# Kernel optimization log

Measured on AMD Instinct MI355X. Metric: run time of the kernel, lower is better.

## Reference

```python
import jax, jax.numpy as jnp
import numpy as np


def setup_inputs() -> dict:
    key = jax.random.key(0)
    ks = jax.random.split(key, 5)
    B, N, C = 64, 384, 768
    return {
        "x": jax.random.normal(ks[0], (B, N, C), dtype=jnp.float32),
        "x_hsi": jax.random.normal(ks[1], (B, N, C), dtype=jnp.float32),
        "qkv_w": jax.random.normal(ks[2], (3 * C, C), dtype=jnp.float32) * 0.02,
        "proj_w": jax.random.normal(ks[3], (C, C), dtype=jnp.float32) * 0.02,
        "proj_b": jax.random.normal(ks[4], (C,), dtype=jnp.float32) * 0.02,
        "t_h": 8,
        "t_w": 8,
        "s_h": 16,
        "s_w": 16,
        "num_heads": 12,
    }


def reference(x, x_hsi, qkv_w, proj_w, proj_b, t_h, t_w, s_h, s_w, num_heads):
    B, N, C = x.shape
    H = num_heads
    Dh = C // H
    scale = Dh ** -0.5
    Lt = t_h * t_w * 2  # template tokens (2 templates)

    def qkv_heads(inp):
        qkv = (inp @ qkv_w.T).reshape(B, N, 3, H, Dh)
        qkv = jnp.transpose(qkv, (2, 0, 3, 1, 4))  # [3,B,H,N,Dh]
        return qkv[0], qkv[1], qkv[2]

    q, k, v = qkv_heads(x)
    q_hsi, k_hsi, v_hsi = qkv_heads(x_hsi)

    q_mt, q_s = q[:, :, :Lt], q[:, :, Lt:]
    k_mt, v_mt = k[:, :, :Lt], v[:, :, :Lt]
    q_s_hsi = q_hsi[:, :, Lt:]

    def attn(qq, kk, vv):
        a = jax.nn.softmax(jnp.einsum('bhqd,bhkd->bhqk', qq, kk) * scale, axis=-1)
        o = jnp.einsum('bhqk,bhkd->bhqd', a, vv)
        return jnp.transpose(o, (0, 2, 1, 3)).reshape(B, -1, C)

    x_mt = attn(q_mt, k_mt, v_mt)        # template-template
    x_s = attn(q_s, k, v)                # search attends to all
    x_s_hsi = attn(q_s_hsi, k_hsi, v_hsi)  # hsi search attends to all hsi

    out = jnp.concatenate([x_mt, x_s], axis=1) @ proj_w.T + proj_b
    out_hsi = jnp.concatenate([x_mt, x_s_hsi], axis=1) @ proj_w.T + proj_b
    return out, out_hsi
```

## Files before the change

kernel.cpp:

```cpp
#include <hip/hip_runtime.h>

typedef __attribute__((ext_vector_type(8))) short short8;
typedef __attribute__((ext_vector_type(4))) short bf16x4;
typedef __attribute__((ext_vector_type(4))) float f32x4;

__device__ __forceinline__ f32x4 mfma16(short8 a, short8 b, f32x4 c) {
  return __builtin_amdgcn_mfma_f32_16x16x32_bf16(a, b, c, 0, 0, 0);
}

__device__ __forceinline__ short f2bf(float f) {
  union { float f; unsigned u; } v; v.f = f;
  unsigned r = (v.u + 0x7fffu + ((v.u >> 16) & 1u)) >> 16;
  return (short)r;
}

__device__ __forceinline__ void gload16(const short* g, short* l) {
  __builtin_amdgcn_global_load_lds(
      (const __attribute__((address_space(1))) void*)g,
      (__attribute__((address_space(3))) void*)l, 16, 0, 0);
}

__global__ __launch_bounds__(256) void cvt_k(const float* __restrict__ src,
                                             short* __restrict__ dst, long n8) {
  long i = (long)blockIdx.x * 256 + threadIdx.x;
  const long stride = (long)gridDim.x * 256;
  for (; i < n8; i += stride) {
    float4 a = *(const float4*)(src + i * 8);
    float4 b = *(const float4*)(src + i * 8 + 4);
    short8 o = {f2bf(a.x), f2bf(a.y), f2bf(a.z), f2bf(a.w),
                f2bf(b.x), f2bf(b.y), f2bf(b.z), f2bf(b.w)};
    *(short8*)(dst + i * 8) = o;
  }
}

__global__ __launch_bounds__(256) void gemm_qkv_k(
    const short* __restrict__ A0, const short* __restrict__ A1,
    const short* __restrict__ W,
    short* __restrict__ O0, short* __restrict__ O1) {
  __shared__ __align__(16) short As[128 * 32];
  __shared__ __align__(16) short Bs[128 * 32];
  const int tid = threadIdx.x;
  const int lane = tid & 63, wv = tid >> 6;
  const int l15 = lane & 15, q4 = lane >> 4;
  const int m0 = blockIdx.x * 128, n0 = blockIdx.y * 128;
  const short* A = blockIdx.z ? A1 : A0;
  short* O = blockIdx.z ? O1 : O0;
  const int wm = wv & 1, wn = wv >> 1;

  const int s0 = tid, s1 = tid + 256;
  const long ga0 = (long)(m0 + (s0 >> 2)) * 768 + (s0 & 3) * 8;
  const long ga1 = (long)(m0 + (s1 >> 2)) * 768 + (s1 & 3) * 8;
  const long gb0 = (long)(n0 + (s0 >> 2)) * 768 + (s0 & 3) * 8;
  const long gb1 = (long)(n0 + (s1 >> 2)) * 768 + (s1 & 3) * 8;
  short* lA0 = &As[(wv * 64) * 8];
  short* lA1 = &As[(wv * 64 + 256) * 8];
  short* lB0 = &Bs[(wv * 64) * 8];
  short* lB1 = &Bs[(wv * 64 + 256) * 8];

  f32x4 acc[4][4] = {};
  for (int k0 = 0; k0 < 768; k0 += 32) {
    __syncthreads();
    gload16(A + ga0 + k0, lA0);
    gload16(A + ga1 + k0, lA1);
    gload16(W + gb0 + k0, lB0);
    gload16(W + gb1 + k0, lB1);
    __syncthreads();
    short8 af[4], bf[4];
#pragma unroll
    for (int i = 0; i < 4; ++i)
      af[i] = *(const short8*)&As[(wm * 64 + i * 16 + l15) * 32 + q4 * 8];
#pragma unroll
    for (int j = 0; j < 4; ++j)
      bf[j] = *(const short8*)&Bs[(wn * 64 + j * 16 + l15) * 32 + q4 * 8];
#pragma unroll
    for (int i = 0; i < 4; ++i)
#pragma unroll
      for (int j = 0; j < 4; ++j)
        acc[i][j] = mfma16(af[i], bf[j], acc[i][j]);
  }
#pragma unroll
  for (int i = 0; i < 4; ++i)
#pragma unroll
    for (int j = 0; j < 4; ++j) {
      const int col = n0 + wn * 64 + j * 16 + l15;
#pragma unroll
      for (int r = 0; r < 4; ++r) {
        const int row = m0 + wm * 64 + i * 16 + q4 * 4 + r;
        O[(long)row * 2304 + col] = f2bf(acc[i][j][r]);
      }
    }
}

template <int NK>
__global__ __launch_bounds__(256) void attn_k(
    const short* __restrict__ qkvx, const short* __restrict__ qkvh,
    short* __restrict__ omt, short* __restrict__ os, short* __restrict__ osh) {
  constexpr int NT = NK / 16;
  constexpr int KT = NK / 64;
  constexpr int T = (NK == 128) ? 2 : 8;
  __shared__ __align__(16) short kv[2][64 * 72];
  __shared__ __align__(16) short sp[2][4][16 * 72];

  const int tid = threadIdx.x, lane = tid & 63, wv = tid >> 6;
  const int l15 = lane & 15, q4 = lane >> 4;
  const int bx = blockIdx.x;
  const int b = bx / (12 * T);
  const int rr = bx % (12 * T);
  const int h = rr / T, t = rr % T;

  const short* src;
  short* outb;
  int q0;
  if (NK == 128) {
    src = qkvx;
    outb = omt + ((long)b * 128 + t * 64) * 768 + h * 64;
    q0 = t * 64;
  } else {
    const int tt = t & 3;
    const bool hs = t >= 4;
    src = hs ? qkvh : qkvx;
    outb = (hs ? osh : os) + ((long)b * 256 + tt * 64) * 768 + h * 64;
    q0 = 128 + tt * 64;
  }
  const short* qb = src + ((long)(b * 384 + q0 + wv * 16)) * 2304 + h * 64;
  const short* kb = src + (long)b * 384 * 2304 + 768 + h * 64;
  const short* vb = kb + 768;

  const int key0 = tid >> 3, dg0 = tid & 7;
  const int key1 = key0 + 32, dg1 = dg0;

  short8 qf0 = *(const short8*)(qb + (long)l15 * 2304 + q4 * 8);
  short8 qf1 = *(const short8*)(qb + (long)l15 * 2304 + 32 + q4 * 8);

  f32x4 sacc[NT] = {};
  short8 ka0 = *(const short8*)(kb + (long)key0 * 2304 + dg0 * 8);
  short8 ka1 = *(const short8*)(kb + (long)key1 * 2304 + dg1 * 8);
#pragma unroll
  for (int kt = 0; kt < KT; ++kt) {
    const int buf = kt & 1;
    *(short8*)&kv[buf][key0 * 72 + dg0 * 8] = ka0;
    *(short8*)&kv[buf][key1 * 72 + dg1 * 8] = ka1;
    __syncthreads();
    if (kt + 1 < KT) {
      ka0 = *(const short8*)(kb + (long)((kt + 1) * 64 + key0) * 2304 + dg0 * 8);
      ka1 = *(const short8*)(kb + (long)((kt + 1) * 64 + key1) * 2304 + dg1 * 8);
    }
#pragma unroll
    for (int j = 0; j < 4; ++j) {
      short8 kf0 = *(const short8*)&kv[buf][(j * 16 + l15) * 72 + q4 * 8];
      short8 kf1 = *(const short8*)&kv[buf][(j * 16 + l15) * 72 + 32 + q4 * 8];
      sacc[kt * 4 + j] = mfma16(qf0, kf0, sacc[kt * 4 + j]);
      sacc[kt * 4 + j] = mfma16(qf1, kf1, sacc[kt * 4 + j]);
    }
  }

  short8 va0 = *(const short8*)(vb + (long)key0 * 2304 + dg0 * 8);
  short8 va1 = *(const short8*)(vb + (long)key1 * 2304 + dg1 * 8);

  const float scale = 0.125f;
  float mx[4] = {-3e38f, -3e38f, -3e38f, -3e38f};
#pragma unroll
  for (int nt = 0; nt < NT; ++nt)
#pragma unroll
    for (int r = 0; r < 4; ++r) mx[r] = fmaxf(mx[r], sacc[nt][r]);
#pragma unroll
  for (int r = 0; r < 4; ++r) {
    mx[r] = fmaxf(mx[r], __shfl_xor(mx[r], 1));
    mx[r] = fmaxf(mx[r], __shfl_xor(mx[r], 2));
    mx[r] = fmaxf(mx[r], __shfl_xor(mx[r], 4));
    mx[r] = fmaxf(mx[r], __shfl_xor(mx[r], 8));
  }
  float sm[4] = {0.f, 0.f, 0.f, 0.f};
  unsigned pb[NT][2];
#pragma unroll
  for (int nt = 0; nt < NT; ++nt) {
    float ev[4];
#pragma unroll
    for (int r = 0; r < 4; ++r) {
      ev[r] = __expf((sacc[nt][r] - mx[r]) * scale);
      sm[r] += ev[r];
    }
    pb[nt][0] = (unsigned)(unsigned short)f2bf(ev[0]) |
                ((unsigned)(unsigned short)f2bf(ev[1]) << 16);
    pb[nt][1] = (unsigned)(unsigned short)f2bf(ev[2]) |
                ((unsigned)(unsigned short)f2bf(ev[3]) << 16);
  }
#pragma unroll
  for (int r = 0; r < 4; ++r) {
    sm[r] += __shfl_xor(sm[r], 1);
    sm[r] += __shfl_xor(sm[r], 2);
    sm[r] += __shfl_xor(sm[r], 4);
    sm[r] += __shfl_xor(sm[r], 8);
  }

  f32x4 oacc[4] = {};
#pragma unroll
  for (int kt = 0; kt < KT; ++kt) {
    const int buf = kt & 1;
    char* vt = (char*)&kv[buf][0];
#pragma unroll
    for (int e = 0; e < 8; ++e) {
      const int d0 = dg0 * 8 + e;
      *(short*)(vt + ((d0 * 144 + key0 * 2) ^ (dg0 << 4))) = va0[e];
      *(short*)(vt + ((d0 * 144 + key1 * 2) ^ (dg1 << 4))) = va1[e];
    }
    short* spw = &sp[buf][wv][0];
#pragma unroll
    for (int nt2 = 0; nt2 < 4; ++nt2) {
#pragma unroll
      for (int p = 0; p < 2; ++p) {
        const unsigned w = pb[kt * 4 + nt2][p];
        spw[(q4 * 4 + 2 * p) * 72 + nt2 * 16 + l15] = (short)(w & 0xffffu);
        spw[(q4 * 4 + 2 * p + 1) * 72 + nt2 * 16 + l15] = (short)(w >> 16);
      }
    }
    __syncthreads();
    if (kt + 1 < KT) {
      va0 = *(const short8*)(vb + (long)((kt + 1) * 64 + key0) * 2304 + dg0 * 8);
      va1 = *(const short8*)(vb + (long)((kt + 1) * 64 + key1) * 2304 + dg1 * 8);
    }
#pragma unroll
    for (int ks = 0; ks < 2; ++ks) {
      short8 pf = *(const short8*)&sp[buf][wv][l15 * 72 + ks * 32 + q4 * 8];
#pragma unroll
      for (int n2 = 0; n2 < 4; ++n2) {
        const int db = n2 * 16 + l15;
        short8 vf = *(const short8*)(vt + ((db * 144 + (ks * 32 + q4 * 8) * 2) ^
                                           (((db >> 3) & 7) << 4)));
        oacc[n2] = mfma16(pf, vf, oacc[n2]);
      }
    }
  }

  short* ob = outb + wv * 16 * 768;
#pragma unroll
  for (int r = 0; r < 4; ++r) {
    const float inv = 1.f / sm[r];
#pragma unroll
    for (int n2 = 0; n2 < 4; ++n2)
      ob[(q4 * 4 + r) * 768 + n2 * 16 + l15] = f2bf(oacc[n2][r] * inv);
  }
}

__global__ __launch_bounds__(256) void gemm_proj_k(
    const short* __restrict__ mt, const short* __restrict__ sA,
    const short* __restrict__ sh,
    const short* __restrict__ W, const float* __restrict__ bias,
    float* __restrict__ out, int cb0) {
  __shared__ __align__(16) short As[128 * 32];
  __shared__ __align__(16) short Bs[128 * 32];
  const int tid = threadIdx.x;
  const int lane = tid & 63, wv = tid >> 6;
  const int l15 = lane & 15, q4 = lane >> 4;
  const int m0 = blockIdx.x * 128, n0 = blockIdx.y * 128;
  const short* s = blockIdx.z ? sh : sA;
  const int wm = wv & 1, wn = wv >> 1;

  const int s0 = tid, s1 = tid + 256;
  const int r0 = s0 >> 2, c0 = (s0 & 3) * 8;
  const int r1 = s1 >> 2, c1 = (s1 & 3) * 8;
  const int ra = m0 + r0, rb = m0 + r1;
  const int ba_ = ra / 384, na = ra % 384;
  const int bb_ = rb / 384, nb = rb % 384;
  const short* ap0 = ((na < 128) ? (mt + ((long)ba_ * 128 + na) * 768)
                                 : (s + ((long)ba_ * 256 + (na - 128)) * 768)) + c0;
  const short* ap1 = ((nb < 128) ? (mt + ((long)bb_ * 128 + nb) * 768)
                                 : (s + ((long)bb_ * 256 + (nb - 128)) * 768)) + c1;
  const short* bp0 = W + (long)(n0 + r0) * 768 + c0;
  const short* bp1 = W + (long)(n0 + r1) * 768 + c1;
  short* lA0 = &As[(wv * 64) * 8];
  short* lA1 = &As[(wv * 64 + 256) * 8];
  short* lB0 = &Bs[(wv * 64) * 8];
  short* lB1 = &Bs[(wv * 64 + 256) * 8];

  f32x4 acc[4][4] = {};
  for (int k0 = 0; k0 < 768; k0 += 32) {
    __syncthreads();
    gload16(ap0 + k0, lA0);
    gload16(ap1 + k0, lA1);
    gload16(bp0 + k0, lB0);
    gload16(bp1 + k0, lB1);
    __syncthreads();
    short8 af[4], bf[4];
#pragma unroll
    for (int i = 0; i < 4; ++i)
      af[i] = *(const short8*)&As[(wm * 64 + i * 16 + l15) * 32 + q4 * 8];
#pragma unroll
    for (int j = 0; j < 4; ++j)
      bf[j] = *(const short8*)&Bs[(wn * 64 + j * 16 + l15) * 32 + q4 * 8];
#pragma unroll
    for (int i = 0; i < 4; ++i)
#pragma unroll
      for (int j = 0; j < 4; ++j)
        acc[i][j] = mfma16(af[i], bf[j], acc[i][j]);
  }
#pragma unroll
  for (int j = 0; j < 4; ++j) {
    const int col = n0 + wn * 64 + j * 16 + l15;
    const float bvv = bias[col];
#pragma unroll
    for (int i = 0; i < 4; ++i)
#pragma unroll
      for (int r = 0; r < 4; ++r) {
        const int row = m0 + wm * 64 + i * 16 + q4 * 4 + r;
        out[(long)blockIdx.z * 18874368 + ((long)cb0 * 384 + row) * 768 + col] =
            acc[i][j][r] + bvv;
      }
  }
}

extern "C" void kernel_launch(void* const* d_in, const int* in_sizes, int n_in,
                              void* d_out, int out_size, void* d_ws, size_t ws_size,
                              hipStream_t stream) {
  (void)in_sizes; (void)n_in; (void)out_size;
  const float* x  = (const float*)d_in[0];
  const float* xh = (const float*)d_in[1];
  const float* qw = (const float*)d_in[2];
  const float* pw = (const float*)d_in[3];
  const float* pb = (const float*)d_in[4];
  float* out = (float*)d_out;

  const long qwSz = 2304L * 768 * 2;
  const long pwSz = 768L * 768 * 2;
  const long fixedW = qwSz + pwSz;
  const long perBatch = (2L * 384 * 768 + 2L * 384 * 2304 + 640L * 768) * 2;
  int CB = 64;
  while (CB > 1 && (long)CB * perBatch + fixedW > (long)ws_size) CB >>= 1;

  char* ws = (char*)d_ws;
  short* qwbf = (short*)ws;
  short* pwbf = (short*)(ws + qwSz);
  char* dyn = ws + fixedW;
  const long xbfSz = (long)CB * 384 * 768 * 2;
  const long qkvSz = (long)CB * 384 * 2304 * 2;
  const long mtSz  = (long)CB * 128 * 768 * 2;
  const long sSz   = (long)CB * 256 * 768 * 2;
  short* xbf  = (short*)dyn;
  short* xhbf = (short*)(dyn + xbfSz);
  short* qkvx = (short*)(dyn + 2 * xbfSz);
  short* qkvh = (short*)(dyn + 2 * xbfSz + qkvSz);
  short* amt  = (short*)(dyn + 2 * xbfSz + 2 * qkvSz);
  short* as_  = (short*)(dyn + 2 * xbfSz + 2 * qkvSz + mtSz);
  short* ash  = (short*)(dyn + 2 * xbfSz + 2 * qkvSz + mtSz + sSz);

  cvt_k<<<864, 256, 0, stream>>>(qw, qwbf, 2304L * 768 / 8);
  cvt_k<<<288, 256, 0, stream>>>(pw, pwbf, 768L * 768 / 8);

  const int nch = 64 / CB;
  for (int c = 0; c < nch; ++c) {
    const int cb0 = c * CB;
    const long n8 = (long)CB * 384 * 768 / 8;
    cvt_k<<<2048, 256, 0, stream>>>(x + (long)cb0 * 384 * 768, xbf, n8);
    cvt_k<<<2048, 256, 0, stream>>>(xh + (long)cb0 * 384 * 768, xhbf, n8);
    dim3 g1(CB * 3, 18, 2);
    gemm_qkv_k<<<g1, 256, 0, stream>>>(xbf, xhbf, qwbf, qkvx, qkvh);
    attn_k<128><<<CB * 12 * 2, 256, 0, stream>>>(qkvx, qkvh, amt, as_, ash);
    attn_k<384><<<CB * 12 * 8, 256, 0, stream>>>(qkvx, qkvh, amt, as_, ash);
    dim3 g3(CB * 3, 6, 2);
    gemm_proj_k<<<g3, 256, 0, stream>>>(amt, as_, ash, pwbf, pb, out, cb0);
  }
}
```

Baseline: 755.2 us.

## Use 256x256 double-buffered swizzled LDS GEMM core for QKV and projection

Replaces the 128x128 single-buffered GEMM loops with a shared 256x256 tile core run by 512 threads. It double-buffers 128KB of dynamic LDS with an XOR swizzle and issues prefetches of the next k-tile between MFMA phases, using s_setprio around the MFMA bursts. The aim is more data reuse per load, fewer bank conflicts, and global-load latency hidden behind compute. The cost is heavy register and LDS use, so only one block fits per CU, and the grid is coarser, which can leave tail imbalance.

```diff
diff --git a/kernel.cpp b/kernel.cpp
--- a/kernel.cpp
+++ b/kernel.cpp
@@ -33,60 +33,160 @@
   }
 }
 
-__global__ __launch_bounds__(256) void gemm_qkv_k(
+__device__ __forceinline__ void gemm256_core(
+    const short* a00, const short* a01, const short* a10, const short* a11,
+    const short* b00, const short* b01, const short* b10, const short* b11,
+    char* lds, int wv, int lane, f32x4 (&acc)[8][4]) {
+  const int l15 = lane & 15, q4 = lane >> 4;
+  const int wm = wv & 1, wn = wv >> 1;
+  const char* rdA = lds + wm * 16384;
+  const char* rdB = lds + 32768 + (wn >> 1) * 16384;
+  const int rB0 = (wn & 1) * 64;
+
+  auto stg = [&](int T, int h, int tt) {
+    const int t = tt >= 12 ? tt - 12 : tt;
+    char* d = lds + (t & 1) * 65536 + T * 32768 + h * 16384 + wv * 2048;
+    const short* g0 = T ? (h ? b10 : b00) : (h ? a10 : a00);
+    const short* g1 = T ? (h ? b11 : b01) : (h ? a11 : a01);
+    gload16(g0 + t * 64, (short*)d);
+    gload16(g1 + t * 64, (short*)(d + 1024));
+  };
+  auto rdfrag = [&](const char* base, int rowl, int ks) -> short8 {
+    int off = ks * 8192 + rowl * 64 + q4 * 16;
+    off ^= ((off >> 9) & 1) << 5;
+    return *(const short8*)(base + off);
+  };
+
+  stg(0, 0, 0); stg(0, 1, 0); stg(1, 0, 0); stg(1, 1, 0);
+  stg(1, 0, 1); stg(1, 1, 1);
+  asm volatile("s_waitcnt vmcnt(4)" ::: "memory");
+  __builtin_amdgcn_s_barrier();
+
+  auto ktile = [&](int buf, int t) {
+    const char* A = rdA + buf * 65536;
+    const char* B = rdB + buf * 65536;
+    short8 af[4][2], bfr[4][2];
+#pragma unroll
+    for (int m = 0; m < 4; ++m) {
+      af[m][0] = rdfrag(A, m * 16 + l15, 0);
+      af[m][1] = rdfrag(A, m * 16 + l15, 1);
+    }
+#pragma unroll
+    for (int n = 0; n < 2; ++n) {
+      bfr[n][0] = rdfrag(B, rB0 + n * 16 + l15, 0);
+      bfr[n][1] = rdfrag(B, rB0 + n * 16 + l15, 1);
+    }
+    stg(0, 0, t + 1);
+    __builtin_amdgcn_s_barrier();
+    __builtin_amdgcn_s_setprio(1);
+#pragma unroll
+    for (int m = 0; m < 4; ++m)
+#pragma unroll
+      for (int n = 0; n < 2; ++n) {
+        acc[m][n] = mfma16(af[m][0], bfr[n][0], acc[m][n]);
+        acc[m][n] = mfma16(af[m][1], bfr[n][1], acc[m][n]);
+      }
+    __builtin_amdgcn_s_setprio(0);
+    __builtin_amdgcn_s_barrier();
+#pragma unroll
+    for (int n = 2; n < 4; ++n) {
+      bfr[n][0] = rdfrag(B, rB0 + n * 16 + l15, 0);
+      bfr[n][1] = rdfrag(B, rB0 + n * 16 + l15, 1);
+    }
+    stg(0, 1, t + 1);
+    __builtin_amdgcn_s_barrier();
+    __builtin_amdgcn_s_setprio(1);
+#pragma unroll
+    for (int m = 0; m < 4; ++m)
+#pragma unroll
+      for (int n = 2; n < 4; ++n) {
+        acc[m][n] = mfma16(af[m][0], bfr[n][0], acc[m][n]);
+        acc[m][n] = mfma16(af[m][1], bfr[n][1], acc[m][n]);
+      }
+    __builtin_amdgcn_s_setprio(0);
+    __builtin_amdgcn_s_barrier();
+#pragma unroll
+    for (int m = 0; m < 4; ++m) {
+      af[m][0] = rdfrag(A, (m + 4) * 16 + l15, 0);
+      af[m][1] = rdfrag(A, (m + 4) * 16 + l15, 1);
+    }
+    stg(1, 0, t + 2);
+    __builtin_amdgcn_s_barrier();
+    __builtin_amdgcn_s_setprio(1);
+#pragma unroll
+    for (int m = 0; m < 4; ++m)
+#pragma unroll
+      for (int n = 0; n < 2; ++n) {
+        acc[m + 4][n] = mfma16(af[m][0], bfr[n][0], acc[m + 4][n]);
+        acc[m + 4][n] = mfma16(af[m][1], bfr[n][1], acc[m + 4][n]);
+      }
+    __builtin_amdgcn_s_setprio(0);
+    __builtin_amdgcn_s_barrier();
+    stg(1, 1, t + 2);
+    __builtin_amdgcn_s_barrier();
+    __builtin_amdgcn_s_setprio(1);
+#pragma unroll
+    for (int m = 0; m < 4; ++m)
+#pragma unroll
+      for (int n = 2; n < 4; ++n) {
+        acc[m + 4][n] = mfma16(af[m][0], bfr[n][0], acc[m + 4][n]);
+        acc[m + 4][n] = mfma16(af[m][1], bfr[n][1], acc[m + 4][n]);
+      }
+    __builtin_amdgcn_s_setprio(0);
+    asm volatile("s_waitcnt vmcnt(4)" ::: "memory");
+    __builtin_amdgcn_s_barrier();
+  };
+
+  for (int g = 0; g < 6; ++g) {
+    ktile(0, 2 * g);
+    ktile(1, 2 * g + 1);
+  }
+}
+
+__device__ __forceinline__ void stage_geom(int wv, int lane, int* srow, int* coff) {
+#pragma unroll
+  for (int j = 0; j < 2; ++j) {
+    const int s = wv * 128 + j * 64 + lane;
+    srow[j] = (s >> 2) & 127;
+    coff[j] = (s >> 9) * 32 + (((((s & 3) << 4) ^ (((s >> 5) & 1) << 5))) >> 1);
+  }
+}
+
+__global__ __launch_bounds__(512, 2) void gemm_qkv_k(
     const short* __restrict__ A0, const short* __restrict__ A1,
     const short* __restrict__ W,
     short* __restrict__ O0, short* __restrict__ O1) {
-  __shared__ __align__(16) short As[128 * 32];
-  __shared__ __align__(16) short Bs[128 * 32];
-  const int tid = threadIdx.x;
-  const int lane = tid & 63, wv = tid >> 6;
+  extern __shared__ char lds[];
+  const int tid = threadIdx.x, lane = tid & 63, wv = tid >> 6;
   const int l15 = lane & 15, q4 = lane >> 4;
-  const int m0 = blockIdx.x * 128, n0 = blockIdx.y * 128;
+  const int m0 = blockIdx.x * 256, n0 = blockIdx.y * 256;
   const short* A = blockIdx.z ? A1 : A0;
   short* O = blockIdx.z ? O1 : O0;
+
+  int srow[2], coff[2];
+  stage_geom(wv, lane, srow, coff);
+  const short* a00 = A + (long)(m0 + srow[0]) * 768 + coff[0];
+  const short* a01 = A + (long)(m0 + srow[1]) * 768 + coff[1];
+  const short* a10 = A + (long)(m0 + 128 + srow[0]) * 768 + coff[0];
+  const short* a11 = A + (long)(m0 + 128 + srow[1]) * 768 + coff[1];
+  const short* b00 = W + (long)(n0 + srow[0]) * 768 + coff[0];
+  const short* b01 = W + (long)(n0 + srow[1]) * 768 + coff[1];
+  const short* b10 = W + (long)(n0 + 128 + srow[0]) * 768 + coff[0];
+  const short* b11 = W + (long)(n0 + 128 + srow[1]) * 768 + coff[1];
+
+  f32x4 acc[8][4] = {};
+  gemm256_core(a00, a01, a10, a11, b00, b01, b10, b11, lds, wv, lane, acc);
+
   const int wm = wv & 1, wn = wv >> 1;
-
-  const int s0 = tid, s1 = tid + 256;
-  const long ga0 = (long)(m0 + (s0 >> 2)) * 768 + (s0 & 3) * 8;
-  const long ga1 = (long)(m0 + (s1 >> 2)) * 768 + (s1 & 3) * 8;
-  const long gb0 = (long)(n0 + (s0 >> 2)) * 768 + (s0 & 3) * 8;
-  const long gb1 = (long)(n0 + (s1 >> 2)) * 768 + (s1 & 3) * 8;
-  short* lA0 = &As[(wv * 64) * 8];
-  short* lA1 = &As[(wv * 64 + 256) * 8];
-  short* lB0 = &Bs[(wv * 64) * 8];
-  short* lB1 = &Bs[(wv * 64 + 256) * 8];
-
-  f32x4 acc[4][4] = {};
-  for (int k0 = 0; k0 < 768; k0 += 32) {
-    __syncthreads();
-    gload16(A + ga0 + k0, lA0);
-    gload16(A + ga1 + k0, lA1);
-    gload16(W + gb0 + k0, lB0);
-    gload16(W + gb1 + k0, lB1);
-    __syncthreads();
-    short8 af[4], bf[4];
-#pragma unroll
-    for (int i = 0; i < 4; ++i)
-      af[i] = *(const short8*)&As[(wm * 64 + i * 16 + l15) * 32 + q4 * 8];
-#pragma unroll
-    for (int j = 0; j < 4; ++j)
-      bf[j] = *(const short8*)&Bs[(wn * 64 + j * 16 + l15) * 32 + q4 * 8];
-#pragma unroll
-    for (int i = 0; i < 4; ++i)
-#pragma unroll
-      for (int j = 0; j < 4; ++j)
-        acc[i][j] = mfma16(af[i], bf[j], acc[i][j]);
-  }
-#pragma unroll
-  for (int i = 0; i < 4; ++i)
-#pragma unroll
-    for (int j = 0; j < 4; ++j) {
-      const int col = n0 + wn * 64 + j * 16 + l15;
+#pragma unroll
+  for (int m = 0; m < 8; ++m)
+#pragma unroll
+    for (int n = 0; n < 4; ++n) {
+      const int col = n0 + wn * 64 + n * 16 + l15;
 #pragma unroll
       for (int r = 0; r < 4; ++r) {
-        const int row = m0 + wm * 64 + i * 16 + q4 * 4 + r;
-        O[(long)row * 2304 + col] = f2bf(acc[i][j][r]);
+        const int row = m0 + wm * 128 + m * 16 + q4 * 4 + r;
+        O[(long)row * 2304 + col] = f2bf(acc[m][n][r]);
       }
     }
 }
@@ -242,69 +342,48 @@
   }
 }
 
-__global__ __launch_bounds__(256) void gemm_proj_k(
+__global__ __launch_bounds__(512, 2) void gemm_proj_k(
     const short* __restrict__ mt, const short* __restrict__ sA,
     const short* __restrict__ sh,
     const short* __restrict__ W, const float* __restrict__ bias,
     float* __restrict__ out, int cb0) {
-  __shared__ __align__(16) short As[128 * 32];
-  __shared__ __align__(16) short Bs[128 * 32];
-  const int tid = threadIdx.x;
-  const int lane = tid & 63, wv = tid >> 6;
+  extern __shared__ char lds[];
+  const int tid = threadIdx.x, lane = tid & 63, wv = tid >> 6;
   const int l15 = lane & 15, q4 = lane >> 4;
-  const int m0 = blockIdx.x * 128, n0 = blockIdx.y * 128;
+  const int m0 = blockIdx.x * 256, n0 = blockIdx.y * 256;
   const short* s = blockIdx.z ? sh : sA;
+
+  int srow[2], coff[2];
+  stage_geom(wv, lane, srow, coff);
+  auto arow = [&](int r) -> const short* {
+    const int ba = r / 384, na = r % 384;
+    return na < 128 ? (mt + ((long)ba * 128 + na) * 768)
+                    : (s + ((long)ba * 256 + (na - 128)) * 768);
+  };
+  const short* a00 = arow(m0 + srow[0]) + coff[0];
+  const short* a01 = arow(m0 + srow[1]) + coff[1];
+  const short* a10 = arow(m0 + 128 + srow[0]) + coff[0];
+  const short* a11 = arow(m0 + 128 + srow[1]) + coff[1];
+  const short* b00 = W + (long)(n0 + srow[0]) * 768 + coff[0];
+  const short* b01 = W + (long)(n0 + srow[1]) * 768 + coff[1];
+  const short* b10 = W + (long)(n0 + 128 + srow[0]) * 768 + coff[0];
+  const short* b11 = W + (long)(n0 + 128 + srow[1]) * 768 + coff[1];
+
+  f32x4 acc[8][4] = {};
+  gemm256_core(a00, a01, a10, a11, b00, b01, b10, b11, lds, wv, lane, acc);
+
   const int wm = wv & 1, wn = wv >> 1;
-
-  const int s0 = tid, s1 = tid + 256;
-  const int r0 = s0 >> 2, c0 = (s0 & 3) * 8;
-  const int r1 = s1 >> 2, c1 = (s1 & 3) * 8;
-  const int ra = m0 + r0, rb = m0 + r1;
-  const int ba_ = ra / 384, na = ra % 384;
-  const int bb_ = rb / 384, nb = rb % 384;
-  const short* ap0 = ((na < 128) ? (mt + ((long)ba_ * 128 + na) * 768)
-                                 : (s + ((long)ba_ * 256 + (na - 128)) * 768)) + c0;
-  const short* ap1 = ((nb < 128) ? (mt + ((long)bb_ * 128 + nb) * 768)
-                                 : (s + ((long)bb_ * 256 + (nb - 128)) * 768)) + c1;
-  const short* bp0 = W + (long)(n0 + r0) * 768 + c0;
-  const short* bp1 = W + (long)(n0 + r1) * 768 + c1;
-  short* lA0 = &As[(wv * 64) * 8];
-  short* lA1 = &As[(wv * 64 + 256) * 8];
-  short* lB0 = &Bs[(wv * 64) * 8];
-  short* lB1 = &Bs[(wv * 64 + 256) * 8];
-
-  f32x4 acc[4][4] = {};
-  for (int k0 = 0; k0 < 768; k0 += 32) {
-    __syncthreads();
-    gload16(ap0 + k0, lA0);
-    gload16(ap1 + k0, lA1);
-    gload16(bp0 + k0, lB0);
-    gload16(bp1 + k0, lB1);
-    __syncthreads();
-    short8 af[4], bf[4];
-#pragma unroll
-    for (int i = 0; i < 4; ++i)
-      af[i] = *(const short8*)&As[(wm * 64 + i * 16 + l15) * 32 + q4 * 8];
-#pragma unroll
-    for (int j = 0; j < 4; ++j)
-      bf[j] = *(const short8*)&Bs[(wn * 64 + j * 16 + l15) * 32 + q4 * 8];
-#pragma unroll
-    for (int i = 0; i < 4; ++i)
-#pragma unroll
-      for (int j = 0; j < 4; ++j)
-        acc[i][j] = mfma16(af[i], bf[j], acc[i][j]);
-  }
-#pragma unroll
-  for (int j = 0; j < 4; ++j) {
-    const int col = n0 + wn * 64 + j * 16 + l15;
+#pragma unroll
+  for (int n = 0; n < 4; ++n) {
+    const int col = n0 + wn * 64 + n * 16 + l15;
     const float bvv = bias[col];
 #pragma unroll
-    for (int i = 0; i < 4; ++i)
+    for (int m = 0; m < 8; ++m)
 #pragma unroll
       for (int r = 0; r < 4; ++r) {
-        const int row = m0 + wm * 64 + i * 16 + q4 * 4 + r;
+        const int row = m0 + wm * 128 + m * 16 + q4 * 4 + r;
         out[(long)blockIdx.z * 18874368 + ((long)cb0 * 384 + row) * 768 + col] =
-            acc[i][j][r] + bvv;
+            acc[m][n][r] + bvv;
       }
   }
 }
@@ -325,7 +404,7 @@
   const long fixedW = qwSz + pwSz;
   const long perBatch = (2L * 384 * 768 + 2L * 384 * 2304 + 640L * 768) * 2;
   int CB = 64;
-  while (CB > 1 && (long)CB * perBatch + fixedW > (long)ws_size) CB >>= 1;
+  while (CB > 2 && (long)CB * perBatch + fixedW > (long)ws_size) CB >>= 1;
 
   char* ws = (char*)d_ws;
   short* qwbf = (short*)ws;
@@ -352,11 +431,11 @@
     const long n8 = (long)CB * 384 * 768 / 8;
     cvt_k<<<2048, 256, 0, stream>>>(x + (long)cb0 * 384 * 768, xbf, n8);
     cvt_k<<<2048, 256, 0, stream>>>(xh + (long)cb0 * 384 * 768, xhbf, n8);
-    dim3 g1(CB * 3, 18, 2);
-    gemm_qkv_k<<<g1, 256, 0, stream>>>(xbf, xhbf, qwbf, qkvx, qkvh);
+    dim3 g1((CB * 384) / 256, 9, 2);
+    gemm_qkv_k<<<g1, 512, 131072, stream>>>(xbf, xhbf, qwbf, qkvx, qkvh);
     attn_k<128><<<CB * 12 * 2, 256, 0, stream>>>(qkvx, qkvh, amt, as_, ash);
     attn_k<384><<<CB * 12 * 8, 256, 0, stream>>>(qkvx, qkvh, amt, as_, ash);
-    dim3 g3(CB * 3, 6, 2);
-    gemm_proj_k<<<g3, 256, 0, stream>>>(amt, as_, ash, pwbf, pb, out, cb0);
-  }
-}
+    dim3 g3((CB * 384) / 256, 3, 2);
+    gemm_proj_k<<<g3, 512, 131072, stream>>>(amt, as_, ash, pwbf, pb, out, cb0);
+  }
+}
```

After: 712.1 us. -5.7%, faster.
